# Performance work log

Hardware: AMD Instinct MI355X
Metric: run time of the kernel (lower is better)

## Reference

```python
import jax, jax.numpy as jnp
import numpy as np

PI = 3.14159265358979323846
MARGIN = 6.0
DIM = 256
ENT_TOT = 43234
REL_RANGE = (6.0 + 2.0) / DIM  # (margin + epsilon) / dim = 0.03125


def setup_inputs() -> dict:
    key = jax.random.key(0)
    k1, k2, k3 = jax.random.split(key, 3)
    head = jax.random.normal(k1, (32, 2 * DIM), dtype=jnp.float32)
    relation = jax.random.normal(k2, (32, DIM), dtype=jnp.float32)
    ent_emb = jax.random.normal(k3, (ENT_TOT, 2 * DIM), dtype=jnp.float32)
    return {"head": head, "relation": relation, "ent_emb": ent_emb}


def reference(head, relation, ent_emb):
    # head: (B, 2D) -> re/im halves (B, D)
    re_h, im_h = jnp.split(head, 2, axis=-1)
    # entity table: (E, 2D) -> (E, D) each
    re_t, im_t = jnp.split(ent_emb, 2, axis=-1)
    # phase rotation from relation embedding
    phase = relation / (REL_RANGE / PI)          # (B, D)
    re_r = jnp.cos(phase)
    im_r = jnp.sin(phase)
    # complex rotation of head by relation: (B, D)
    re_rot = re_h * re_r - im_h * im_r
    im_rot = re_h * im_r + im_h * re_r
    # difference against every entity, broadcast to (B, E, D)
    re_s = re_rot[:, None, :] - re_t[None, :, :]
    im_s = im_rot[:, None, :] - im_t[None, :, :]
    # L2 norm over the complex pair, summed over D -> (B, E)
    dist = jnp.sqrt(re_s * re_s + im_s * im_s).sum(axis=-1)
    return MARGIN - dist
```

## Files before the change

### kernel.cpp

```cpp
#include <hip/hip_runtime.h>
#include <math.h>

#define DIMH 256
#define NB   32
#define E_TOT 43234
#define TE   64
#define DK   32
#define NCHUNK (DIMH / DK)
#define PHASE_DIV 0.009947183943243459f

typedef float v2f __attribute__((ext_vector_type(2)));

__global__ void rot_kernel(const float* __restrict__ head,
                           const float* __restrict__ rel,
                           float* __restrict__ rot) {
    int i = blockIdx.x * blockDim.x + threadIdx.x;
    int b = i >> 8;
    int d = i & 255;
    float re_h = head[b * 2 * DIMH + d];
    float im_h = head[b * 2 * DIMH + DIMH + d];
    float ph = rel[b * DIMH + d] / PHASE_DIV;
    float s, c;
    sincosf(ph, &s, &c);
    rot[b * DIMH + d]             = re_h * c - im_h * s;
    rot[NB * DIMH + b * DIMH + d] = re_h * s + im_h * c;
}

__device__ __forceinline__ v2f sqrt2(v2f s) {
    v2f r;
    r.x = __builtin_amdgcn_sqrtf(s.x);
    r.y = __builtin_amdgcn_sqrtf(s.y);
    return r;
}

__global__ __launch_bounds__(256, 5) void dist_kernel(const float* __restrict__ ent,
                                                      const float* __restrict__ rot,
                                                      float* __restrict__ out) {
    __shared__ float s_er[TE][DK + 2];
    __shared__ float s_ei[TE][DK + 2];
    __shared__ float s_rr[NB][DK + 2];
    __shared__ float s_ri[NB][DK + 2];

    const int tid = threadIdx.x;
    const int eb  = blockIdx.x * TE;
    const int g   = tid & 15;
    const int b0  = (tid >> 4) * 2;

    v2f acc0[4], acc1[4];
    #pragma unroll
    for (int k = 0; k < 4; ++k) {
        acc0[k].x = 0.f; acc0[k].y = 0.f;
        acc1[k].x = 0.f; acc1[k].y = 0.f;
    }

    for (int c = 0; c < NCHUNK; ++c) {
        const int dk = c * DK;
        #pragma unroll
        for (int qq = 0; qq < 2; ++qq) {
            int q   = tid + qq * 256;
            int row = q >> 3;
            int col = (q & 7) << 2;
            int er  = eb + row;
            if (er >= E_TOT) er = E_TOT - 1;
            float4 vre = *reinterpret_cast<const float4*>(&ent[(size_t)er * (2 * DIMH) + dk + col]);
            float4 vim = *reinterpret_cast<const float4*>(&ent[(size_t)er * (2 * DIMH) + DIMH + dk + col]);
            *reinterpret_cast<float2*>(&s_er[row][col])     = make_float2(vre.x, vre.y);
            *reinterpret_cast<float2*>(&s_er[row][col + 2]) = make_float2(vre.z, vre.w);
            *reinterpret_cast<float2*>(&s_ei[row][col])     = make_float2(vim.x, vim.y);
            *reinterpret_cast<float2*>(&s_ei[row][col + 2]) = make_float2(vim.z, vim.w);
        }
        {
            int row = tid >> 3;
            int col = (tid & 7) << 2;
            float4 vrr = *reinterpret_cast<const float4*>(&rot[row * DIMH + dk + col]);
            float4 vri = *reinterpret_cast<const float4*>(&rot[NB * DIMH + row * DIMH + dk + col]);
            *reinterpret_cast<float2*>(&s_rr[row][col])     = make_float2(vrr.x, vrr.y);
            *reinterpret_cast<float2*>(&s_rr[row][col + 2]) = make_float2(vrr.z, vrr.w);
            *reinterpret_cast<float2*>(&s_ri[row][col])     = make_float2(vri.x, vri.y);
            *reinterpret_cast<float2*>(&s_ri[row][col + 2]) = make_float2(vri.z, vri.w);
        }
        __syncthreads();

        #pragma unroll 2
        for (int d = 0; d < DK; d += 2) {
            v2f rr0 = *reinterpret_cast<const v2f*>(&s_rr[b0    ][d]);
            v2f rr1 = *reinterpret_cast<const v2f*>(&s_rr[b0 + 1][d]);
            v2f ri0 = *reinterpret_cast<const v2f*>(&s_ri[b0    ][d]);
            v2f ri1 = *reinterpret_cast<const v2f*>(&s_ri[b0 + 1][d]);
            #pragma unroll
            for (int k = 0; k < 4; ++k) {
                v2f er = *reinterpret_cast<const v2f*>(&s_er[g + 16 * k][d]);
                v2f ei = *reinterpret_cast<const v2f*>(&s_ei[g + 16 * k][d]);
                v2f a0 = rr0 - er, c0 = ri0 - ei;
                v2f a1 = rr1 - er, c1 = ri1 - ei;
                v2f s0 = a0 * a0 + c0 * c0;
                v2f s1 = a1 * a1 + c1 * c1;
                acc0[k] += sqrt2(s0);
                acc1[k] += sqrt2(s1);
            }
        }
        __syncthreads();
    }

    #pragma unroll
    for (int k = 0; k < 4; ++k) {
        int e = eb + g + 16 * k;
        if (e < E_TOT) {
            out[(size_t)b0 * E_TOT + e]       = 6.0f - (acc0[k].x + acc0[k].y);
            out[(size_t)(b0 + 1) * E_TOT + e] = 6.0f - (acc1[k].x + acc1[k].y);
        }
    }
}

extern "C" void kernel_launch(void* const* d_in, const int* in_sizes, int n_in,
                              void* d_out, int out_size, void* d_ws, size_t ws_size,
                              hipStream_t stream) {
    const float* head = (const float*)d_in[0];
    const float* rel  = (const float*)d_in[1];
    const float* ent  = (const float*)d_in[2];
    float* rot = (float*)d_ws;

    rot_kernel<<<(NB * DIMH) / 256, 256, 0, stream>>>(head, rel, rot);

    int nblocks = (E_TOT + TE - 1) / TE;
    dist_kernel<<<nblocks, 256, 0, stream>>>(ent, rot, (float*)d_out);
}
```

Before: 179.8 us.

## Enlarge register tile to 4x4 and split D across blocks with atomics

Each thread now computes a 4x4 batch-by-entity tile instead of 2x4, and the entity tile grows to 128. The reduction dimension is split in half across two blocks, which combine their partial sums with float atomicAdd into an output pre-initialised to the margin by a new init kernel. The larger tile cuts shared-memory loads per sqrt, and the split keeps the block count up. In exchange it adds an extra kernel launch, atomic traffic, more register pressure, and non-deterministic summation order.

```diff
diff --git a/kernel.cpp b/kernel.cpp
--- a/kernel.cpp
+++ b/kernel.cpp
@@ -4,12 +4,20 @@
 #define DIMH 256
 #define NB   32
 #define E_TOT 43234
-#define TE   64
+#define TE   128
 #define DK   32
-#define NCHUNK (DIMH / DK)
+#define DHALF 128
 #define PHASE_DIV 0.009947183943243459f
 
 typedef float v2f __attribute__((ext_vector_type(2)));
+
+__global__ __launch_bounds__(256) void init_kernel(float* __restrict__ out) {
+    int i = blockIdx.x * 256 + threadIdx.x;
+    if (i < (NB * E_TOT) / 4) {
+        float4 v = make_float4(6.0f, 6.0f, 6.0f, 6.0f);
+        reinterpret_cast<float4*>(out)[i] = v;
+    }
+}
 
 __global__ void rot_kernel(const float* __restrict__ head,
                            const float* __restrict__ rel,
@@ -33,7 +41,7 @@
     return r;
 }
 
-__global__ __launch_bounds__(256, 5) void dist_kernel(const float* __restrict__ ent,
+__global__ __launch_bounds__(256, 4) void dist_kernel(const float* __restrict__ ent,
                                                       const float* __restrict__ rot,
                                                       float* __restrict__ out) {
     __shared__ float s_er[TE][DK + 2];
@@ -41,29 +49,32 @@
     __shared__ float s_rr[NB][DK + 2];
     __shared__ float s_ri[NB][DK + 2];
 
-    const int tid = threadIdx.x;
-    const int eb  = blockIdx.x * TE;
-    const int g   = tid & 15;
-    const int b0  = (tid >> 4) * 2;
+    const int tid   = threadIdx.x;
+    const int etile = blockIdx.x >> 1;
+    const int half  = blockIdx.x & 1;
+    const int eb    = etile * TE;
+    const int eg    = tid & 31;
+    const int bg    = (tid >> 5) * 4;
+    const int dbase = half * DHALF;
 
-    v2f acc0[4], acc1[4];
+    v2f acc[4][4];
     #pragma unroll
-    for (int k = 0; k < 4; ++k) {
-        acc0[k].x = 0.f; acc0[k].y = 0.f;
-        acc1[k].x = 0.f; acc1[k].y = 0.f;
-    }
+    for (int j = 0; j < 4; ++j)
+        #pragma unroll
+        for (int k = 0; k < 4; ++k) { acc[j][k].x = 0.f; acc[j][k].y = 0.f; }
 
-    for (int c = 0; c < NCHUNK; ++c) {
-        const int dk = c * DK;
+    for (int c = 0; c < DHALF / DK; ++c) {
+        const int dk = dbase + c * DK;
         #pragma unroll
-        for (int qq = 0; qq < 2; ++qq) {
-            int q   = tid + qq * 256;
+        for (int it = 0; it < 4; ++it) {
+            int q   = tid + it * 256;
             int row = q >> 3;
             int col = (q & 7) << 2;
             int er  = eb + row;
             if (er >= E_TOT) er = E_TOT - 1;
-            float4 vre = *reinterpret_cast<const float4*>(&ent[(size_t)er * (2 * DIMH) + dk + col]);
-            float4 vim = *reinterpret_cast<const float4*>(&ent[(size_t)er * (2 * DIMH) + DIMH + dk + col]);
+            const float* base = &ent[(size_t)er * (2 * DIMH)];
+            float4 vre = *reinterpret_cast<const float4*>(base + dk + col);
+            float4 vim = *reinterpret_cast<const float4*>(base + DIMH + dk + col);
             *reinterpret_cast<float2*>(&s_er[row][col])     = make_float2(vre.x, vre.y);
             *reinterpret_cast<float2*>(&s_er[row][col + 2]) = make_float2(vre.z, vre.w);
             *reinterpret_cast<float2*>(&s_ei[row][col])     = make_float2(vim.x, vim.y);
@@ -83,31 +94,38 @@
 
         #pragma unroll 2
         for (int d = 0; d < DK; d += 2) {
-            v2f rr0 = *reinterpret_cast<const v2f*>(&s_rr[b0    ][d]);
-            v2f rr1 = *reinterpret_cast<const v2f*>(&s_rr[b0 + 1][d]);
-            v2f ri0 = *reinterpret_cast<const v2f*>(&s_ri[b0    ][d]);
-            v2f ri1 = *reinterpret_cast<const v2f*>(&s_ri[b0 + 1][d]);
+            v2f rr[4], ri[4], er[4], ei[4];
+            #pragma unroll
+            for (int j = 0; j < 4; ++j) {
+                rr[j] = *reinterpret_cast<const v2f*>(&s_rr[bg + j][d]);
+                ri[j] = *reinterpret_cast<const v2f*>(&s_ri[bg + j][d]);
+            }
             #pragma unroll
             for (int k = 0; k < 4; ++k) {
-                v2f er = *reinterpret_cast<const v2f*>(&s_er[g + 16 * k][d]);
-                v2f ei = *reinterpret_cast<const v2f*>(&s_ei[g + 16 * k][d]);
-                v2f a0 = rr0 - er, c0 = ri0 - ei;
-                v2f a1 = rr1 - er, c1 = ri1 - ei;
-                v2f s0 = a0 * a0 + c0 * c0;
-                v2f s1 = a1 * a1 + c1 * c1;
-                acc0[k] += sqrt2(s0);
-                acc1[k] += sqrt2(s1);
+                er[k] = *reinterpret_cast<const v2f*>(&s_er[eg + 32 * k][d]);
+                ei[k] = *reinterpret_cast<const v2f*>(&s_ei[eg + 32 * k][d]);
             }
+            #pragma unroll
+            for (int j = 0; j < 4; ++j)
+                #pragma unroll
+                for (int k = 0; k < 4; ++k) {
+                    v2f a = rr[j] - er[k];
+                    v2f b = ri[j] - ei[k];
+                    v2f s = a * a + b * b;
+                    acc[j][k] += sqrt2(s);
+                }
         }
         __syncthreads();
     }
 
     #pragma unroll
     for (int k = 0; k < 4; ++k) {
-        int e = eb + g + 16 * k;
+        int e = eb + eg + 32 * k;
         if (e < E_TOT) {
-            out[(size_t)b0 * E_TOT + e]       = 6.0f - (acc0[k].x + acc0[k].y);
-            out[(size_t)(b0 + 1) * E_TOT + e] = 6.0f - (acc1[k].x + acc1[k].y);
+            #pragma unroll
+            for (int j = 0; j < 4; ++j)
+                atomicAdd(&out[(size_t)(bg + j) * E_TOT + e],
+                          -(acc[j][k].x + acc[j][k].y));
         }
     }
 }
@@ -120,8 +138,10 @@
     const float* ent  = (const float*)d_in[2];
     float* rot = (float*)d_ws;
 
+    int init_blocks = ((NB * E_TOT) / 4 + 255) / 256;
+    init_kernel<<<init_blocks, 256, 0, stream>>>((float*)d_out);
     rot_kernel<<<(NB * DIMH) / 256, 256, 0, stream>>>(head, rel, rot);
 
-    int nblocks = (E_TOT + TE - 1) / TE;
-    dist_kernel<<<nblocks, 256, 0, stream>>>(ent, rot, (float*)d_out);
+    int etiles = (E_TOT + TE - 1) / TE;
+    dist_kernel<<<etiles * 2, 256, 0, stream>>>(ent, rot, (float*)d_out);
 }
```

New measurement: 176.5 us. Within noise of the previous version (-1.8%).

## Shrink entity tile, use float4 shared layout, and prefetch next chunk into registers

Applied to the files above, without the earlier changes.

Cuts the entity tile from 64 to 16 rows per block, so each thread computes 2 batches x 1 entity and the grid grows about fourfold. Shared memory now holds float4 vectors and the inner loop consumes four dims per step. The next chunk's global loads are issued into registers before the current chunk is computed, a software prefetch that overlaps memory latency with compute. In exchange, each thread does much less work per shared-memory load of the relation tile, which is now reloaded per block: 4x more rot traffic and more block overhead.

```diff
diff --git a/kernel.cpp b/kernel.cpp
--- a/kernel.cpp
+++ b/kernel.cpp
@@ -4,111 +4,104 @@
 #define DIMH 256
 #define NB   32
 #define E_TOT 43234
-#define TE   64
+#define TE   16
 #define DK   32
-#define NCHUNK (DIMH / DK)
+#define NC   (DIMH / DK)
 #define PHASE_DIV 0.009947183943243459f
 
-typedef float v2f __attribute__((ext_vector_type(2)));
+typedef float v4f __attribute__((ext_vector_type(4)));
 
-__global__ void rot_kernel(const float* __restrict__ head,
-                           const float* __restrict__ rel,
-                           float* __restrict__ rot) {
-    int i = blockIdx.x * blockDim.x + threadIdx.x;
+__global__ __launch_bounds__(256) void rot_kernel(const float* __restrict__ head,
+                                                  const float* __restrict__ rel,
+                                                  float* __restrict__ rot) {
+    int i = blockIdx.x * 256 + threadIdx.x;
     int b = i >> 8;
     int d = i & 255;
     float re_h = head[b * 2 * DIMH + d];
     float im_h = head[b * 2 * DIMH + DIMH + d];
-    float ph = rel[b * DIMH + d] / PHASE_DIV;
     float s, c;
-    sincosf(ph, &s, &c);
+    sincosf(rel[b * DIMH + d] / PHASE_DIV, &s, &c);
     rot[b * DIMH + d]             = re_h * c - im_h * s;
     rot[NB * DIMH + b * DIMH + d] = re_h * s + im_h * c;
 }
 
-__device__ __forceinline__ v2f sqrt2(v2f s) {
-    v2f r;
+__device__ __forceinline__ v4f sqrt4(v4f s) {
+    v4f r;
     r.x = __builtin_amdgcn_sqrtf(s.x);
     r.y = __builtin_amdgcn_sqrtf(s.y);
+    r.z = __builtin_amdgcn_sqrtf(s.z);
+    r.w = __builtin_amdgcn_sqrtf(s.w);
     return r;
 }
 
-__global__ __launch_bounds__(256, 5) void dist_kernel(const float* __restrict__ ent,
+__global__ __launch_bounds__(256, 6) void dist_kernel(const float* __restrict__ ent,
                                                       const float* __restrict__ rot,
                                                       float* __restrict__ out) {
-    __shared__ float s_er[TE][DK + 2];
-    __shared__ float s_ei[TE][DK + 2];
-    __shared__ float s_rr[NB][DK + 2];
-    __shared__ float s_ri[NB][DK + 2];
+    __shared__ v4f s_er[TE][DK / 4 + 1];
+    __shared__ v4f s_ei[TE][DK / 4 + 1];
+    __shared__ v4f s_rr[NB][DK / 4 + 1];
+    __shared__ v4f s_ri[NB][DK / 4 + 1];
 
     const int tid = threadIdx.x;
     const int eb  = blockIdx.x * TE;
-    const int g   = tid & 15;
-    const int b0  = (tid >> 4) * 2;
+    const int ep  = tid & 15;
+    const int bp  = tid >> 4;
 
-    v2f acc0[4], acc1[4];
-    #pragma unroll
-    for (int k = 0; k < 4; ++k) {
-        acc0[k].x = 0.f; acc0[k].y = 0.f;
-        acc1[k].x = 0.f; acc1[k].y = 0.f;
-    }
+    const int sh   = tid >> 7;
+    const int srow = (tid >> 3) & 15;
+    const int sq   = tid & 7;
+    const int er   = min(eb + srow, E_TOT - 1);
+    const int rrow = tid >> 3;
+    const int rq   = tid & 7;
 
-    for (int c = 0; c < NCHUNK; ++c) {
+    float4 p_e, p_rr, p_ri;
+
+    auto load_chunk = [&](int c) {
         const int dk = c * DK;
-        #pragma unroll
-        for (int qq = 0; qq < 2; ++qq) {
-            int q   = tid + qq * 256;
-            int row = q >> 3;
-            int col = (q & 7) << 2;
-            int er  = eb + row;
-            if (er >= E_TOT) er = E_TOT - 1;
-            float4 vre = *reinterpret_cast<const float4*>(&ent[(size_t)er * (2 * DIMH) + dk + col]);
-            float4 vim = *reinterpret_cast<const float4*>(&ent[(size_t)er * (2 * DIMH) + DIMH + dk + col]);
-            *reinterpret_cast<float2*>(&s_er[row][col])     = make_float2(vre.x, vre.y);
-            *reinterpret_cast<float2*>(&s_er[row][col + 2]) = make_float2(vre.z, vre.w);
-            *reinterpret_cast<float2*>(&s_ei[row][col])     = make_float2(vim.x, vim.y);
-            *reinterpret_cast<float2*>(&s_ei[row][col + 2]) = make_float2(vim.z, vim.w);
-        }
+        p_e  = *reinterpret_cast<const float4*>(&ent[(size_t)er * (2 * DIMH) + sh * DIMH + dk + 4 * sq]);
+        p_rr = *reinterpret_cast<const float4*>(&rot[rrow * DIMH + dk + 4 * rq]);
+        p_ri = *reinterpret_cast<const float4*>(&rot[NB * DIMH + rrow * DIMH + dk + 4 * rq]);
+    };
+
+    v4f acc0, acc1;
+    acc0 = 0.f; acc1 = 0.f;
+
+    load_chunk(0);
+
+    for (int c = 0; c < NC; ++c) {
         {
-            int row = tid >> 3;
-            int col = (tid & 7) << 2;
-            float4 vrr = *reinterpret_cast<const float4*>(&rot[row * DIMH + dk + col]);
-            float4 vri = *reinterpret_cast<const float4*>(&rot[NB * DIMH + row * DIMH + dk + col]);
-            *reinterpret_cast<float2*>(&s_rr[row][col])     = make_float2(vrr.x, vrr.y);
-            *reinterpret_cast<float2*>(&s_rr[row][col + 2]) = make_float2(vrr.z, vrr.w);
-            *reinterpret_cast<float2*>(&s_ri[row][col])     = make_float2(vri.x, vri.y);
-            *reinterpret_cast<float2*>(&s_ri[row][col + 2]) = make_float2(vri.z, vri.w);
+            v4f e; e.x = p_e.x; e.y = p_e.y; e.z = p_e.z; e.w = p_e.w;
+            (sh ? s_ei : s_er)[srow][sq] = e;
+            v4f r0; r0.x = p_rr.x; r0.y = p_rr.y; r0.z = p_rr.z; r0.w = p_rr.w;
+            v4f r1; r1.x = p_ri.x; r1.y = p_ri.y; r1.z = p_ri.z; r1.w = p_ri.w;
+            s_rr[rrow][rq] = r0;
+            s_ri[rrow][rq] = r1;
         }
         __syncthreads();
 
-        #pragma unroll 2
-        for (int d = 0; d < DK; d += 2) {
-            v2f rr0 = *reinterpret_cast<const v2f*>(&s_rr[b0    ][d]);
-            v2f rr1 = *reinterpret_cast<const v2f*>(&s_rr[b0 + 1][d]);
-            v2f ri0 = *reinterpret_cast<const v2f*>(&s_ri[b0    ][d]);
-            v2f ri1 = *reinterpret_cast<const v2f*>(&s_ri[b0 + 1][d]);
-            #pragma unroll
-            for (int k = 0; k < 4; ++k) {
-                v2f er = *reinterpret_cast<const v2f*>(&s_er[g + 16 * k][d]);
-                v2f ei = *reinterpret_cast<const v2f*>(&s_ei[g + 16 * k][d]);
-                v2f a0 = rr0 - er, c0 = ri0 - ei;
-                v2f a1 = rr1 - er, c1 = ri1 - ei;
-                v2f s0 = a0 * a0 + c0 * c0;
-                v2f s1 = a1 * a1 + c1 * c1;
-                acc0[k] += sqrt2(s0);
-                acc1[k] += sqrt2(s1);
-            }
+        if (c + 1 < NC) load_chunk(c + 1);
+
+        #pragma unroll 4
+        for (int q = 0; q < DK / 4; ++q) {
+            v4f rr0 = s_rr[2 * bp][q];
+            v4f rr1 = s_rr[2 * bp + 1][q];
+            v4f ri0 = s_ri[2 * bp][q];
+            v4f ri1 = s_ri[2 * bp + 1][q];
+            v4f ere = s_er[ep][q];
+            v4f eim = s_ei[ep][q];
+
+            {   v4f a = rr0 - ere, b = ri0 - eim;
+                acc0 += sqrt4(a * a + b * b); }
+            {   v4f a = rr1 - ere, b = ri1 - eim;
+                acc1 += sqrt4(a * a + b * b); }
         }
         __syncthreads();
     }
 
-    #pragma unroll
-    for (int k = 0; k < 4; ++k) {
-        int e = eb + g + 16 * k;
-        if (e < E_TOT) {
-            out[(size_t)b0 * E_TOT + e]       = 6.0f - (acc0[k].x + acc0[k].y);
-            out[(size_t)(b0 + 1) * E_TOT + e] = 6.0f - (acc1[k].x + acc1[k].y);
-        }
+    const int e = eb + ep;
+    if (e < E_TOT) {
+        out[(size_t)(2 * bp) * E_TOT + e]     = 6.0f - (acc0.x + acc0.y + acc0.z + acc0.w);
+        out[(size_t)(2 * bp + 1) * E_TOT + e] = 6.0f - (acc1.x + acc1.y + acc1.z + acc1.w);
     }
 }
 
@@ -122,6 +115,6 @@
 
     rot_kernel<<<(NB * DIMH) / 256, 256, 0, stream>>>(head, rel, rot);
 
-    int nblocks = (E_TOT + TE - 1) / TE;
-    dist_kernel<<<nblocks, 256, 0, stream>>>(ent, rot, (float*)d_out);
+    int etiles = (E_TOT + TE - 1) / TE;
+    dist_kernel<<<etiles, 256, 0, stream>>>(ent, rot, (float*)d_out);
 }
```

After: 178.0 us. Within noise of the previous version (-1.0%).
